# Performance work log

Hardware: AMD Instinct MI355X
Metric: run time of the kernel (lower is better)

Reference implementation:

```python
import jax, jax.numpy as jnp
import numpy as np

NUM_HEAD = 8


def setup_inputs() -> dict:
    key = jax.random.key(0)
    k1, k2, k3, k4 = jax.random.split(key, 4)
    B, C, H, W = 16, 512, 64, 64
    x = jax.random.normal(k1, (B, C, H, W), dtype=jnp.float32)
    w_qkv = jax.random.normal(k2, (3 * C, C), dtype=jnp.float32) * 0.02  # Conv2d 1x1, no bias
    w_proj = jax.random.normal(k3, (C, C), dtype=jnp.float32) * 0.02
    b_proj = jax.random.normal(k4, (C,), dtype=jnp.float32) * 0.02
    return {"x": x, "w_qkv": w_qkv, "w_proj": w_proj, "b_proj": b_proj}


def reference(x, w_qkv, w_proj, b_proj):
    B, C, H, W = x.shape
    nh = NUM_HEAD
    hd = C // nh
    scale = hd ** (-0.5)
    # 1x1 conv == channel matmul
    qkv = jnp.einsum('oc,bchw->bohw', w_qkv, x)  # [B, 3C, H, W]
    q, k, v = jnp.split(qkv, 3, axis=1)
    q = q.reshape(B, nh, hd, H * W)
    k = k.reshape(B, nh, hd, H * W)
    v = v.reshape(B, nh, hd, H * W)
    # NOTE: faithful to source: contracts over the spatial (last) axis,
    # producing a [B, nh, hd, hd] matrix.
    attn = jnp.einsum('bnqd,bnkd->bnqk', q, k) * scale
    attn = jax.nn.softmax(attn, axis=-1)
    # Faithful to source: 'k' and 'v' are both summed independently (outer sum),
    # exactly as torch.einsum computes it.
    out = jnp.einsum('bnqk,bnvd->bnqd', attn, v)
    out = out.reshape(B, C, H, W)
    return jnp.einsum('oc,bchw->bohw', w_proj, out) + b_proj[None, :, None, None]
```

## Files before the change

kernel.cpp:

```cpp
#include <hip/hip_runtime.h>

#define CDIM 512
#define NH 8
#define HWDIM 4096
#define BATCH 16
#define PTILE 256
#define PSTRIDE (BATCH * NH * HWDIM)

__global__ __launch_bounds__(256) void prep_kernel(
    const float* __restrict__ wqkv, const float* __restrict__ wproj,
    float* __restrict__ wvT, float* __restrict__ wp) {
  int idx = blockIdx.x * 256 + threadIdx.x;
  if (idx < 4096) {
    int n = idx >> 9, c = idx & 511;
    const float* p = wqkv + (size_t)(1024 + n * 64) * CDIM + c;
    float s = 0.f;
#pragma unroll 8
    for (int j = 0; j < 64; ++j) s += p[(size_t)j * CDIM];
    wvT[c * 8 + n] = s;
  } else if (idx < 8192) {
    int i2 = idx - 4096;
    int n = i2 >> 9, o = i2 & 511;
    const float* p = wproj + (size_t)o * CDIM + n * 64;
    float s = 0.f;
#pragma unroll 4
    for (int j = 0; j < 16; ++j) {
      float4 v = *(const float4*)(p + j * 4);
      s += v.x + v.y + v.z + v.w;
    }
    wp[o * 8 + n] = s;
  }
}

__global__ __launch_bounds__(256, 4) void s_part_kernel(
    const float* __restrict__ x, const float* __restrict__ wvT,
    float* __restrict__ pS) {
  __shared__ __align__(16) float sPart[4][NH][PTILE];

  const int t = threadIdx.x;
  const int wave = t >> 6;
  const int lane = t & 63;
  const int bx = blockIdx.x;
  const int pt = bx & 255;
  const int cg = bx >> 8;
  const int b = pt >> 4;
  const int hw0 = (pt & 15) << 8;

  const int c0 = cg * 128 + wave * 32;
  const float* xb = x + ((size_t)b * CDIM + c0) * HWDIM + hw0 + lane * 4;
  const float* wb = wvT + c0 * 8;

  float acc[NH][4];
#pragma unroll
  for (int n = 0; n < NH; ++n)
    acc[n][0] = acc[n][1] = acc[n][2] = acc[n][3] = 0.f;

#pragma unroll 8
  for (int cc = 0; cc < 32; ++cc) {
    const float4 xv = *(const float4*)(xb + (size_t)cc * HWDIM);
    const float4 w0 = *(const float4*)(wb + cc * 8);
    const float4 w1 = *(const float4*)(wb + cc * 8 + 4);
    const float wn[8] = {w0.x, w0.y, w0.z, w0.w, w1.x, w1.y, w1.z, w1.w};
    const float xv4[4] = {xv.x, xv.y, xv.z, xv.w};
#pragma unroll
    for (int n = 0; n < NH; ++n)
#pragma unroll
      for (int p = 0; p < 4; ++p) acc[n][p] = fmaf(wn[n], xv4[p], acc[n][p]);
  }

#pragma unroll
  for (int n = 0; n < NH; ++n)
    *(float4*)&sPart[wave][n][lane * 4] =
        make_float4(acc[n][0], acc[n][1], acc[n][2], acc[n][3]);
  __syncthreads();

  float* out = pS + (size_t)cg * PSTRIDE + ((size_t)b * NH) * HWDIM + hw0;
#pragma unroll
  for (int r = 0; r < 8; ++r) {
    const int i = t + r * 256;
    const int n = i >> 8, sp = i & 255;
    const float v =
        sPart[0][n][sp] + sPart[1][n][sp] + sPart[2][n][sp] + sPart[3][n][sp];
    out[(size_t)n * HWDIM + sp] = v;
  }
}

__global__ __launch_bounds__(256, 4) void y_kernel(
    const float* __restrict__ pS, const float* __restrict__ wp,
    const float* __restrict__ bias, float* __restrict__ y) {
  const int t = threadIdx.x;
  const int wave = t >> 6;
  const int lane = t & 63;
  const int bx = blockIdx.x;
  const int pt = bx & 255;
  const int og = bx >> 8;
  const int b = pt >> 4;
  const int hw0 = (pt & 15) << 8;

  float4 Sv[NH];
#pragma unroll
  for (int n = 0; n < NH; ++n) {
    const float* p = pS + ((size_t)b * NH + n) * HWDIM + hw0 + lane * 4;
    const float4 a0 = *(const float4*)(p);
    const float4 a1 = *(const float4*)(p + PSTRIDE);
    const float4 a2 = *(const float4*)(p + 2 * (size_t)PSTRIDE);
    const float4 a3 = *(const float4*)(p + 3 * (size_t)PSTRIDE);
    Sv[n] = make_float4(a0.x + a1.x + a2.x + a3.x, a0.y + a1.y + a2.y + a3.y,
                        a0.z + a1.z + a2.z + a3.z, a0.w + a1.w + a2.w + a3.w);
  }

  const int o0 = og * 128 + wave * 32;
  const float* wb = wp + o0 * 8;
  const float* bb = bias + o0;
  float* yb = y + ((size_t)b * CDIM + o0) * HWDIM + hw0 + lane * 4;

#pragma unroll 4
  for (int i = 0; i < 32; ++i) {
    const float4 w0 = *(const float4*)(wb + i * 8);
    const float4 w1 = *(const float4*)(wb + i * 8 + 4);
    const float wn[8] = {w0.x, w0.y, w0.z, w0.w, w1.x, w1.y, w1.z, w1.w};
    const float b0 = bb[i];
    float r[4] = {b0, b0, b0, b0};
#pragma unroll
    for (int n = 0; n < NH; ++n) {
      r[0] = fmaf(wn[n], Sv[n].x, r[0]);
      r[1] = fmaf(wn[n], Sv[n].y, r[1]);
      r[2] = fmaf(wn[n], Sv[n].z, r[2]);
      r[3] = fmaf(wn[n], Sv[n].w, r[3]);
    }
    *(float4*)(yb + (size_t)i * HWDIM) = make_float4(r[0], r[1], r[2], r[3]);
  }
}

extern "C" void kernel_launch(void* const* d_in, const int* in_sizes, int n_in,
                              void* d_out, int out_size, void* d_ws, size_t ws_size,
                              hipStream_t stream) {
  const float* x     = (const float*)d_in[0];
  const float* wqkv  = (const float*)d_in[1];
  const float* wproj = (const float*)d_in[2];
  const float* bproj = (const float*)d_in[3];
  float* y = (float*)d_out;

  float* wvT = (float*)d_ws;
  float* wp  = wvT + 4096;
  float* pS  = wp + 4096;

  prep_kernel<<<32, 256, 0, stream>>>(wqkv, wproj, wvT, wp);
  s_part_kernel<<<1024, 256, 0, stream>>>(x, wvT, pS);
  y_kernel<<<1024, 256, 0, stream>>>(pS, wp, bproj, y);
}
```

Measured before the change: 280.8 us.

## Give each thread full channel group, drop LDS reduction, shrink grids to 256 blocks

Each thread now walks all 128 channels of its group rather than 32, which removes the shared-memory cross-wave reduction in the S kernel. Each thread covers 4 spatial positions across 1024-wide tiles, and the grid drops from 1024 to 256 blocks for both the S and Y kernels. It adds batched 8-deep x loads and __syncthreads calls inside the loops, apparently to keep waves in step. The risk is that only 256 blocks may underfill the GPU and cut memory-level parallelism for what is a bandwidth-bound workload.

```diff
diff --git a/kernel.cpp b/kernel.cpp
--- a/kernel.cpp
+++ b/kernel.cpp
@@ -4,8 +4,7 @@
 #define NH 8
 #define HWDIM 4096
 #define BATCH 16
-#define PTILE 256
-#define PSTRIDE (BATCH * NH * HWDIM)
+#define PSTRIDE ((size_t)BATCH * NH * HWDIM)
 
 __global__ __launch_bounds__(256) void prep_kernel(
     const float* __restrict__ wqkv, const float* __restrict__ wproj,
@@ -32,103 +31,101 @@
   }
 }
 
-__global__ __launch_bounds__(256, 4) void s_part_kernel(
+__global__ __launch_bounds__(256) void s_part_kernel(
     const float* __restrict__ x, const float* __restrict__ wvT,
     float* __restrict__ pS) {
-  __shared__ __align__(16) float sPart[4][NH][PTILE];
+  const int t = threadIdx.x;
+  const int bx = blockIdx.x;
+  const int pt = bx & 63;
+  const int cg = bx >> 6;
+  const int b = pt >> 2;
+  const int s0 = ((pt & 3) << 10) + t * 4;
 
-  const int t = threadIdx.x;
-  const int wave = t >> 6;
-  const int lane = t & 63;
-  const int bx = blockIdx.x;
-  const int pt = bx & 255;
-  const int cg = bx >> 8;
-  const int b = pt >> 4;
-  const int hw0 = (pt & 15) << 8;
-
-  const int c0 = cg * 128 + wave * 32;
-  const float* xb = x + ((size_t)b * CDIM + c0) * HWDIM + hw0 + lane * 4;
-  const float* wb = wvT + c0 * 8;
+  const float* xb = x + ((size_t)b * CDIM + cg * 128) * HWDIM + s0;
+  const float* wb = wvT + cg * 128 * 8;
 
   float acc[NH][4];
 #pragma unroll
   for (int n = 0; n < NH; ++n)
     acc[n][0] = acc[n][1] = acc[n][2] = acc[n][3] = 0.f;
 
-#pragma unroll 8
-  for (int cc = 0; cc < 32; ++cc) {
-    const float4 xv = *(const float4*)(xb + (size_t)cc * HWDIM);
-    const float4 w0 = *(const float4*)(wb + cc * 8);
-    const float4 w1 = *(const float4*)(wb + cc * 8 + 4);
-    const float wn[8] = {w0.x, w0.y, w0.z, w0.w, w1.x, w1.y, w1.z, w1.w};
-    const float xv4[4] = {xv.x, xv.y, xv.z, xv.w};
+  for (int cc0 = 0; cc0 < 128; cc0 += 16) {
 #pragma unroll
-    for (int n = 0; n < NH; ++n)
+    for (int half = 0; half < 2; ++half) {
+      float4 xv[8];
 #pragma unroll
-      for (int p = 0; p < 4; ++p) acc[n][p] = fmaf(wn[n], xv4[p], acc[n][p]);
+      for (int u = 0; u < 8; ++u)
+        xv[u] = *(const float4*)(xb + (size_t)(cc0 + half * 8 + u) * HWDIM);
+#pragma unroll
+      for (int u = 0; u < 8; ++u) {
+        const int c = cc0 + half * 8 + u;
+        const float4 w0 = *(const float4*)(wb + c * 8);
+        const float4 w1 = *(const float4*)(wb + c * 8 + 4);
+        const float wn[8] = {w0.x, w0.y, w0.z, w0.w, w1.x, w1.y, w1.z, w1.w};
+        const float xv4[4] = {xv[u].x, xv[u].y, xv[u].z, xv[u].w};
+#pragma unroll
+        for (int n = 0; n < NH; ++n)
+#pragma unroll
+          for (int p = 0; p < 4; ++p)
+            acc[n][p] = fmaf(wn[n], xv4[p], acc[n][p]);
+      }
+    }
+    __syncthreads();
   }
 
+  float* out = pS + (size_t)cg * PSTRIDE + ((size_t)b * NH) * HWDIM + s0;
 #pragma unroll
   for (int n = 0; n < NH; ++n)
-    *(float4*)&sPart[wave][n][lane * 4] =
+    *(float4*)(out + (size_t)n * HWDIM) =
         make_float4(acc[n][0], acc[n][1], acc[n][2], acc[n][3]);
-  __syncthreads();
-
-  float* out = pS + (size_t)cg * PSTRIDE + ((size_t)b * NH) * HWDIM + hw0;
-#pragma unroll
-  for (int r = 0; r < 8; ++r) {
-    const int i = t + r * 256;
-    const int n = i >> 8, sp = i & 255;
-    const float v =
-        sPart[0][n][sp] + sPart[1][n][sp] + sPart[2][n][sp] + sPart[3][n][sp];
-    out[(size_t)n * HWDIM + sp] = v;
-  }
 }
 
-__global__ __launch_bounds__(256, 4) void y_kernel(
+__global__ __launch_bounds__(256) void y_kernel(
     const float* __restrict__ pS, const float* __restrict__ wp,
     const float* __restrict__ bias, float* __restrict__ y) {
   const int t = threadIdx.x;
-  const int wave = t >> 6;
-  const int lane = t & 63;
   const int bx = blockIdx.x;
-  const int pt = bx & 255;
-  const int og = bx >> 8;
-  const int b = pt >> 4;
-  const int hw0 = (pt & 15) << 8;
+  const int pt = bx & 63;
+  const int og = bx >> 6;
+  const int b = pt >> 2;
+  const int s0 = ((pt & 3) << 10) + t * 4;
 
   float4 Sv[NH];
+  const float* base = pS + ((size_t)b * NH) * HWDIM + s0;
 #pragma unroll
   for (int n = 0; n < NH; ++n) {
-    const float* p = pS + ((size_t)b * NH + n) * HWDIM + hw0 + lane * 4;
+    const float* p = base + (size_t)n * HWDIM;
     const float4 a0 = *(const float4*)(p);
     const float4 a1 = *(const float4*)(p + PSTRIDE);
-    const float4 a2 = *(const float4*)(p + 2 * (size_t)PSTRIDE);
-    const float4 a3 = *(const float4*)(p + 3 * (size_t)PSTRIDE);
+    const float4 a2 = *(const float4*)(p + 2 * PSTRIDE);
+    const float4 a3 = *(const float4*)(p + 3 * PSTRIDE);
     Sv[n] = make_float4(a0.x + a1.x + a2.x + a3.x, a0.y + a1.y + a2.y + a3.y,
                         a0.z + a1.z + a2.z + a3.z, a0.w + a1.w + a2.w + a3.w);
   }
 
-  const int o0 = og * 128 + wave * 32;
+  const int o0 = og * 128;
   const float* wb = wp + o0 * 8;
   const float* bb = bias + o0;
-  float* yb = y + ((size_t)b * CDIM + o0) * HWDIM + hw0 + lane * 4;
+  float* yb = y + ((size_t)b * CDIM + o0) * HWDIM + s0;
 
-#pragma unroll 4
-  for (int i = 0; i < 32; ++i) {
-    const float4 w0 = *(const float4*)(wb + i * 8);
-    const float4 w1 = *(const float4*)(wb + i * 8 + 4);
-    const float wn[8] = {w0.x, w0.y, w0.z, w0.w, w1.x, w1.y, w1.z, w1.w};
-    const float b0 = bb[i];
-    float r[4] = {b0, b0, b0, b0};
+  for (int i0 = 0; i0 < 128; i0 += 32) {
+#pragma unroll 8
+    for (int i = i0; i < i0 + 32; ++i) {
+      const float4 w0 = *(const float4*)(wb + i * 8);
+      const float4 w1 = *(const float4*)(wb + i * 8 + 4);
+      const float wn[8] = {w0.x, w0.y, w0.z, w0.w, w1.x, w1.y, w1.z, w1.w};
+      const float b0 = bb[i];
+      float r[4] = {b0, b0, b0, b0};
 #pragma unroll
-    for (int n = 0; n < NH; ++n) {
-      r[0] = fmaf(wn[n], Sv[n].x, r[0]);
-      r[1] = fmaf(wn[n], Sv[n].y, r[1]);
-      r[2] = fmaf(wn[n], Sv[n].z, r[2]);
-      r[3] = fmaf(wn[n], Sv[n].w, r[3]);
+      for (int n = 0; n < NH; ++n) {
+        r[0] = fmaf(wn[n], Sv[n].x, r[0]);
+        r[1] = fmaf(wn[n], Sv[n].y, r[1]);
+        r[2] = fmaf(wn[n], Sv[n].z, r[2]);
+        r[3] = fmaf(wn[n], Sv[n].w, r[3]);
+      }
+      *(float4*)(yb + (size_t)i * HWDIM) = make_float4(r[0], r[1], r[2], r[3]);
     }
-    *(float4*)(yb + (size_t)i * HWDIM) = make_float4(r[0], r[1], r[2], r[3]);
+    __syncthreads();
   }
 }
 
@@ -146,6 +143,6 @@
   float* pS  = wp + 4096;
 
   prep_kernel<<<32, 256, 0, stream>>>(wqkv, wproj, wvT, wp);
-  s_part_kernel<<<1024, 256, 0, stream>>>(x, wvT, pS);
-  y_kernel<<<1024, 256, 0, stream>>>(pS, wp, bproj, y);
+  s_part_kernel<<<256, 256, 0, stream>>>(x, wvT, pS);
+  y_kernel<<<256, 256, 0, stream>>>(pS, wp, bproj, y);
 }
```

Result: no change. 279.9 us (-0.3%).
